# Performance work log

Measured on AMD Instinct MI355X. Metric: run time of the kernel, lower is better.

Reference implementation:

```python
import jax, jax.numpy as jnp
import numpy as np

COMMITMENT_COST = 0.25


def setup_inputs() -> dict:
    key = jax.random.key(0)
    k1, k2 = jax.random.split(key)
    x = jax.random.normal(k1, (32, 256, 32, 32), dtype=jnp.float32)          # NCHW latents
    embedding = jax.random.normal(k2, (1024, 256), dtype=jnp.float32)        # [K, D] codebook
    return {"x": x, "embedding": embedding}


def reference(x, embedding):
    # NCHW -> NHWC, flatten to [N, D]
    inp = jnp.transpose(x, (0, 2, 3, 1))
    B, H, W, D = inp.shape
    K = embedding.shape[0]
    flat = inp.reshape(-1, D)                                                # [N, D]

    dists = (jnp.sum(flat * flat, axis=1, keepdims=True)
             + jnp.sum(embedding * embedding, axis=1)
             - 2.0 * flat @ embedding.T)
    idx = jnp.argmin(dists, axis=1)                                          # [N]
    encodings = jax.nn.one_hot(idx, K, dtype=flat.dtype)                     # [N, K]

    quantized = (encodings @ embedding).reshape(B, H, W, D)

    # commitment loss (codebook detached, eval path: no EMA update)
    e_latent_loss = jnp.mean(jnp.square(jax.lax.stop_gradient(quantized) - inp))
    loss = COMMITMENT_COST * e_latent_loss

    # straight-through estimator
    quantized_st = inp + jax.lax.stop_gradient(quantized - inp)

    avg_probs = jnp.mean(encodings, axis=0)
    perplexity = jnp.exp(-jnp.sum(avg_probs * jnp.log(avg_probs + 1e-10)))

    return (loss, jnp.transpose(quantized_st, (0, 3, 1, 2)), perplexity, encodings)
```

## Files before the change

kernel.cpp:

```cpp
#include <hip/hip_runtime.h>
#include <math.h>

#define D    256
#define K    1024
#define HWX  1024
#define NPTS 32768
#define PT   64
#define NCHUNK 64

#define Q_OFF    1
#define PERP_OFF (1 + 8388608)
#define ENC_OFF  (2 + 8388608)

#define WS_FRAG_OFF 147456

typedef __attribute__((ext_vector_type(8))) short bf16x8;
typedef __attribute__((ext_vector_type(4))) float f32x4;
typedef __attribute__((ext_vector_type(2))) float f32x2;

__device__ __forceinline__ unsigned short bf16_rne(float f) {
  unsigned int u = __float_as_uint(f);
  u = u + 0x7fffu + ((u >> 16) & 1u);
  return (unsigned short)(u >> 16);
}

#define CONV(F, H, L)                                                          \
  {                                                                            \
    H = bf16_rne(F);                                                           \
    const float fh_ = __uint_as_float((unsigned)(H) << 16);                    \
    L = bf16_rne((F)-fh_);                                                     \
  }

__global__ __launch_bounds__(256) void vq_frag(const float* __restrict__ emb,
                                               unsigned int* __restrict__ frag,
                                               float* __restrict__ enorm,
                                               int* __restrict__ counts,
                                               float* __restrict__ loss_accum) {
  const int gid = blockIdx.x * 256 + threadIdx.x;
  const int c = gid >> 5, g = gid & 31;
  const float* src = emb + (size_t)c * D + g * 8;
  const float4 a = *(const float4*)src;
  const float4 b = *(const float4*)(src + 4);
  float s = a.x * a.x + a.y * a.y + a.z * a.z + a.w * a.w +
            b.x * b.x + b.y * b.y + b.z * b.z + b.w * b.w;
#pragma unroll
  for (int off = 1; off < 32; off <<= 1) s += __shfl_xor(s, off);
  if (g == 0) enorm[c] = s;
  unsigned short h0, h1, h2, h3, h4, h5, h6, h7;
  unsigned short l0, l1, l2, l3, l4, l5, l6, l7;
  CONV(a.x, h0, l0) CONV(a.y, h1, l1) CONV(a.z, h2, l2) CONV(a.w, h3, l3)
  CONV(b.x, h4, l4) CONV(b.y, h5, l5) CONV(b.z, h6, l6) CONV(b.w, h7, l7)
  uint4 uh, ul;
  uh.x = (unsigned)h0 | ((unsigned)h1 << 16); uh.y = (unsigned)h2 | ((unsigned)h3 << 16);
  uh.z = (unsigned)h4 | ((unsigned)h5 << 16); uh.w = (unsigned)h6 | ((unsigned)h7 << 16);
  ul.x = (unsigned)l0 | ((unsigned)l1 << 16); ul.y = (unsigned)l2 | ((unsigned)l3 << 16);
  ul.z = (unsigned)l4 | ((unsigned)l5 << 16); ul.w = (unsigned)l6 | ((unsigned)l7 << 16);
  const int fragidx = (c >> 4) * 16 + (g >> 2) * 2;
  const int Lo = ((c & 15) + 16 * (g & 3)) * 4;
  *(uint4*)(frag + (size_t)fragidx * 256 + Lo) = uh;
  *(uint4*)(frag + (size_t)(fragidx + 1) * 256 + Lo) = ul;
  if (gid < K) counts[gid] = 0;
  if (gid == 0) *loss_accum = 0.0f;
}

#define ISSUE_CHUNK(P, SEL)                                                    \
  {                                                                            \
    const unsigned* gsrc = fragg + (size_t)(P)*4096 + t * 4;                   \
    unsigned short* ldst = fbuf + (SEL)*8192 + t * 8;                          \
    _Pragma("unroll") for (int q = 0; q < 4; ++q)                              \
        __builtin_amdgcn_global_load_lds(                                      \
            (const __attribute__((address_space(1))) unsigned*)(gsrc + q * 1024), \
            (__attribute__((address_space(3))) unsigned*)(ldst + q * 2048),    \
            16, 0, 0);                                                         \
  }

#define AHOIST(KSv)                                                            \
  ah##KSv = *(const bf16x8*)&fbuf[((w * 4 + ((KSv)&3)) * 2 + 0) * 512 + lane * 8]; \
  al##KSv = *(const bf16x8*)&fbuf[((w * 4 + ((KSv)&3)) * 2 + 1) * 512 + lane * 8];

#define KS3(KSv)                                                               \
  {                                                                            \
    const bf16x8 bh = *(const bf16x8*)&fbuf[bufo + ((KSv)*2 + 0) * 512 + lane * 8]; \
    const bf16x8 bl = *(const bf16x8*)&fbuf[bufo + ((KSv)*2 + 1) * 512 + lane * 8]; \
    acc = __builtin_amdgcn_mfma_f32_16x16x32_bf16(ah##KSv, bh, acc, 0, 0, 0);  \
    acc = __builtin_amdgcn_mfma_f32_16x16x32_bf16(al##KSv, bh, acc, 0, 0, 0);  \
    acc = __builtin_amdgcn_mfma_f32_16x16x32_bf16(ah##KSv, bl, acc, 0, 0, 0);  \
  }

#define COMPUTE_CHUNK(P, BUFO)                                                 \
  {                                                                            \
    const int bufo = (BUFO);                                                   \
    f32x4 acc = {0.f, 0.f, 0.f, 0.f};                                          \
    KS3(0) KS3(1) KS3(2) KS3(3) KS3(4) KS3(5) KS3(6) KS3(7)                    \
    const int code = (P)*16 + (lane & 15);                                     \
    const float en_l = en_s[code];                                             \
    float m;                                                                   \
    m = en_l - 2.0f * acc[0]; if (m < mv[0]) { mv[0] = m; mi[0] = code; }      \
    m = en_l - 2.0f * acc[1]; if (m < mv[1]) { mv[1] = m; mi[1] = code; }      \
    m = en_l - 2.0f * acc[2]; if (m < mv[2]) { mv[2] = m; mi[2] = code; }      \
    m = en_l - 2.0f * acc[3]; if (m < mv[3]) { mv[3] = m; mi[3] = code; }      \
  }

#define ENC_ZERO(P)                                                            \
  {                                                                            \
    const f32x2 z_ = {0.f, 0.f};                                               \
    __builtin_nontemporal_store(z_, encz + (P)*512 + t);                       \
    __builtin_nontemporal_store(z_, encz + (P)*512 + 256 + t);                 \
  }

#define CFENCE asm volatile("" ::: "memory");

#define STAGE_X(H)                                                             \
  {                                                                            \
    const int pt = t & 63, cb_ = t >> 6;                                       \
    const float* xb = x + (size_t)bb * (D * HWX) + hw0 + pt;                   \
    _Pragma("unroll 8") for (int i = 0; i < 32; ++i) {                         \
      const int c = (H)*128 + cb_ + 4 * i;                                     \
      const float f = xb[(size_t)c * HWX];                                     \
      unsigned short h_, l_;                                                   \
      CONV(f, h_, l_)                                                          \
      xn_acc += f * f;                                                         \
      const int ksl = (c >> 5) & 3, quad = (c >> 3) & 3, j = c & 7;            \
      const int base =                                                         \
          (((pt >> 4) * 4 + ksl) * 2) * 512 + ((pt & 15) + 16 * quad) * 8 + j; \
      fbuf[base] = h_;                                                         \
      fbuf[base + 512] = l_;                                                   \
    }                                                                          \
  }

__global__ __launch_bounds__(256) void vq_main(const float* __restrict__ x,
                                               const unsigned int* __restrict__ fragg,
                                               const float* __restrict__ emb,
                                               const float* __restrict__ enorm,
                                               float* __restrict__ out_q,
                                               float* __restrict__ out_enc,
                                               float* __restrict__ loss_accum,
                                               int* __restrict__ counts) {
  __shared__ __align__(16) unsigned short fbuf[24576];
  __shared__ float en_s[K];
  __shared__ float xn_part[256];
  __shared__ float val_s[PT];
  __shared__ int idx_s[PT];

  const int t = threadIdx.x;
  const int lane = t & 63;
  const int w = t >> 6;
  const int p0 = blockIdx.x * PT;
  const int bb = p0 >> 10;
  const int hw0 = p0 & 1023;

  bf16x8 ah0, ah1, ah2, ah3, ah4, ah5, ah6, ah7;
  bf16x8 al0, al1, al2, al3, al4, al5, al6, al7;
  float xn_acc = 0.0f;

  STAGE_X(0)
  for (int i = t; i < K; i += 256) en_s[i] = enorm[i];
  __syncthreads();
  AHOIST(0) AHOIST(1) AHOIST(2) AHOIST(3)
  __syncthreads();
  STAGE_X(1)
  xn_part[t] = xn_acc;
  __syncthreads();
  AHOIST(4) AHOIST(5) AHOIST(6) AHOIST(7)
  __syncthreads();

  float mv[4];
  int mi[4];
#pragma unroll
  for (int i = 0; i < 4; ++i) { mv[i] = 3.4e38f; mi[i] = 0; }

  f32x2* encz = reinterpret_cast<f32x2*>(out_enc + (size_t)p0 * K);

  ISSUE_CHUNK(0, 0)
  CFENCE
  ISSUE_CHUNK(1, 1)
  asm volatile("s_waitcnt vmcnt(4)" ::: "memory");
  __builtin_amdgcn_s_barrier();
  CFENCE
  ENC_ZERO(0)
  CFENCE
  ISSUE_CHUNK(2, 2)
  CFENCE
  COMPUTE_CHUNK(0, 0)
  int cb = 1;
  for (int p = 1; p < NCHUNK - 1; ++p) {
    asm volatile("s_waitcnt vmcnt(6)" ::: "memory");
    __builtin_amdgcn_s_barrier();
    CFENCE
    ENC_ZERO(p)
    CFENCE
    if (p + 2 < NCHUNK) {
      ISSUE_CHUNK(p + 2, cb == 0 ? 2 : cb - 1)
    }
    CFENCE
    COMPUTE_CHUNK(p, cb * 8192)
    cb = cb == 2 ? 0 : cb + 1;
  }
  asm volatile("s_waitcnt vmcnt(2)" ::: "memory");
  __builtin_amdgcn_s_barrier();
  CFENCE
  ENC_ZERO(63)
  COMPUTE_CHUNK(63, 0)

#pragma unroll
  for (int off = 1; off < 16; off <<= 1) {
#pragma unroll
    for (int i = 0; i < 4; ++i) {
      const float ov = __shfl_xor(mv[i], off);
      const int oi = __shfl_xor(mi[i], off);
      if (ov < mv[i] || (ov == mv[i] && oi < mi[i])) { mv[i] = ov; mi[i] = oi; }
    }
  }
  if ((lane & 15) == 0) {
    const int quad = lane >> 4;
#pragma unroll
    for (int i = 0; i < 4; ++i) {
      val_s[w * 16 + quad * 4 + i] = mv[i];
      idx_s[w * 16 + quad * 4 + i] = mi[i];
    }
  }
  asm volatile("s_waitcnt vmcnt(0)" ::: "memory");
  __syncthreads();

  float dist = 0.0f;
  if (t < PT) {
    float xn = 0.0f;
#pragma unroll
    for (int g = 0; g < 4; ++g) xn += xn_part[t + 64 * g];
    dist = val_s[t] + xn;
    atomicAdd(&counts[idx_s[t]], 1);
    out_enc[(size_t)(p0 + t) * K + idx_s[t]] = 1.0f;
  }
  if (t < 64) {
#pragma unroll
    for (int off = 32; off > 0; off >>= 1) dist += __shfl_down(dist, off);
    if (t == 0) atomicAdd(loss_accum, dist);
  }

  float* xq = (float*)fbuf;
  for (int qd = 0; qd < 4; ++qd) {
    __syncthreads();
#pragma unroll
    for (int rr = 0; rr < 4; ++rr) {
      const int r = w * 4 + rr;
      const float4 v = ((const float4*)(emb + (size_t)idx_s[qd * 16 + r] * D))[lane];
      float* dst = &xq[r * 257 + lane];
      dst[0] = v.x; dst[64] = v.y; dst[128] = v.z; dst[192] = v.w;
    }
    __syncthreads();
    const int pt = t & 15;
    float* qb = out_q + (size_t)bb * D * HWX + hw0 + qd * 16 + pt;
#pragma unroll
    for (int ii = 0; ii < 16; ++ii) {
      const int ci = (t >> 4) + 16 * ii;
      const int pos = (ci >> 2) + 64 * (ci & 3);
      qb[(size_t)ci * HWX] = xq[pt * 257 + pos];
    }
  }
}

__global__ __launch_bounds__(256) void vq_final(const int* __restrict__ counts,
                                                const float* __restrict__ loss_accum,
                                                float* __restrict__ out) {
  __shared__ float sh[4];
  const int t = threadIdx.x;
  float s = 0.0f;
  for (int k = t; k < K; k += 256) {
    const float p = (float)counts[k] * (1.0f / 32768.0f);
    s += p * logf(p + 1e-10f);
  }
#pragma unroll
  for (int off = 32; off > 0; off >>= 1) s += __shfl_down(s, off);
  if ((t & 63) == 0) sh[t >> 6] = s;
  __syncthreads();
  if (t == 0) {
    const float tot = sh[0] + sh[1] + sh[2] + sh[3];
    out[PERP_OFF] = expf(-tot);
    out[0] = 0.25f * (*loss_accum) / 8388608.0f;
  }
}

extern "C" void kernel_launch(void* const* d_in, const int* in_sizes, int n_in,
                              void* d_out, int out_size, void* d_ws, size_t ws_size,
                              hipStream_t stream) {
  const float* x = (const float*)d_in[0];
  const float* emb = (const float*)d_in[1];
  float* out = (float*)d_out;
  float* enorm = (float*)d_ws;
  int* counts = (int*)((char*)d_ws + 4096);
  float* loss_accum = (float*)((char*)d_ws + 8192);
  unsigned int* fragg = (unsigned int*)((char*)d_ws + WS_FRAG_OFF);

  hipLaunchKernelGGL(vq_frag, dim3(128), dim3(256), 0, stream,
                     emb, fragg, enorm, counts, loss_accum);
  hipLaunchKernelGGL(vq_main, dim3(NPTS / PT), dim3(256), 0, stream,
                     x, fragg, emb, enorm, out + Q_OFF, out + ENC_OFF,
                     loss_accum, counts);
  hipLaunchKernelGGL(vq_final, dim3(1), dim3(256), 0, stream,
                     counts, loss_accum, out);
}
```

Baseline: 264.0 us.

## Halve block to two waves, each computing two 16-point tiles per B fragment

The main kernel now runs 128 threads (2 waves) per block instead of 256. Each wave owns two 16-point A tiles and reuses every codebook B fragment loaded from LDS for both tiles, interleaving two accumulators. This halves the LDS B-fragment reads per MFMA and adds independent MFMA chains. The cost is twice the A registers per thread and fewer waves to hide latency. The staging, prefetch, zeroing and epilogue loops and the vmcnt waits are rescaled to match.

```diff
diff --git a/kernel.cpp b/kernel.cpp
--- a/kernel.cpp
+++ b/kernel.cpp
@@ -67,45 +67,57 @@
   {                                                                            \
     const unsigned* gsrc = fragg + (size_t)(P)*4096 + t * 4;                   \
     unsigned short* ldst = fbuf + (SEL)*8192 + t * 8;                          \
-    _Pragma("unroll") for (int q = 0; q < 4; ++q)                              \
+    _Pragma("unroll") for (int q = 0; q < 8; ++q)                              \
         __builtin_amdgcn_global_load_lds(                                      \
-            (const __attribute__((address_space(1))) unsigned*)(gsrc + q * 1024), \
-            (__attribute__((address_space(3))) unsigned*)(ldst + q * 2048),    \
+            (const __attribute__((address_space(1))) unsigned*)(gsrc + q * 512), \
+            (__attribute__((address_space(3))) unsigned*)(ldst + q * 1024),    \
             16, 0, 0);                                                         \
   }
 
-#define AHOIST(KSv)                                                            \
-  ah##KSv = *(const bf16x8*)&fbuf[((w * 4 + ((KSv)&3)) * 2 + 0) * 512 + lane * 8]; \
-  al##KSv = *(const bf16x8*)&fbuf[((w * 4 + ((KSv)&3)) * 2 + 1) * 512 + lane * 8];
+#define AHOIST2(KSv)                                                           \
+  ahA##KSv = *(const bf16x8*)&fbuf[((tA * 4 + ((KSv)&3)) * 2 + 0) * 512 + lane * 8]; \
+  alA##KSv = *(const bf16x8*)&fbuf[((tA * 4 + ((KSv)&3)) * 2 + 1) * 512 + lane * 8]; \
+  ahB##KSv = *(const bf16x8*)&fbuf[((tB * 4 + ((KSv)&3)) * 2 + 0) * 512 + lane * 8]; \
+  alB##KSv = *(const bf16x8*)&fbuf[((tB * 4 + ((KSv)&3)) * 2 + 1) * 512 + lane * 8];
 
 #define KS3(KSv)                                                               \
   {                                                                            \
     const bf16x8 bh = *(const bf16x8*)&fbuf[bufo + ((KSv)*2 + 0) * 512 + lane * 8]; \
     const bf16x8 bl = *(const bf16x8*)&fbuf[bufo + ((KSv)*2 + 1) * 512 + lane * 8]; \
-    acc = __builtin_amdgcn_mfma_f32_16x16x32_bf16(ah##KSv, bh, acc, 0, 0, 0);  \
-    acc = __builtin_amdgcn_mfma_f32_16x16x32_bf16(al##KSv, bh, acc, 0, 0, 0);  \
-    acc = __builtin_amdgcn_mfma_f32_16x16x32_bf16(ah##KSv, bl, acc, 0, 0, 0);  \
+    accA = __builtin_amdgcn_mfma_f32_16x16x32_bf16(ahA##KSv, bh, accA, 0, 0, 0); \
+    accB = __builtin_amdgcn_mfma_f32_16x16x32_bf16(ahB##KSv, bh, accB, 0, 0, 0); \
+    accA = __builtin_amdgcn_mfma_f32_16x16x32_bf16(alA##KSv, bh, accA, 0, 0, 0); \
+    accB = __builtin_amdgcn_mfma_f32_16x16x32_bf16(alB##KSv, bh, accB, 0, 0, 0); \
+    accA = __builtin_amdgcn_mfma_f32_16x16x32_bf16(ahA##KSv, bl, accA, 0, 0, 0); \
+    accB = __builtin_amdgcn_mfma_f32_16x16x32_bf16(ahB##KSv, bl, accB, 0, 0, 0); \
   }
 
 #define COMPUTE_CHUNK(P, BUFO)                                                 \
   {                                                                            \
     const int bufo = (BUFO);                                                   \
-    f32x4 acc = {0.f, 0.f, 0.f, 0.f};                                          \
+    f32x4 accA = {0.f, 0.f, 0.f, 0.f};                                         \
+    f32x4 accB = {0.f, 0.f, 0.f, 0.f};                                         \
     KS3(0) KS3(1) KS3(2) KS3(3) KS3(4) KS3(5) KS3(6) KS3(7)                    \
     const int code = (P)*16 + (lane & 15);                                     \
     const float en_l = en_s[code];                                             \
     float m;                                                                   \
-    m = en_l - 2.0f * acc[0]; if (m < mv[0]) { mv[0] = m; mi[0] = code; }      \
-    m = en_l - 2.0f * acc[1]; if (m < mv[1]) { mv[1] = m; mi[1] = code; }      \
-    m = en_l - 2.0f * acc[2]; if (m < mv[2]) { mv[2] = m; mi[2] = code; }      \
-    m = en_l - 2.0f * acc[3]; if (m < mv[3]) { mv[3] = m; mi[3] = code; }      \
+    m = en_l - 2.0f * accA[0]; if (m < mvA[0]) { mvA[0] = m; miA[0] = code; }  \
+    m = en_l - 2.0f * accA[1]; if (m < mvA[1]) { mvA[1] = m; miA[1] = code; }  \
+    m = en_l - 2.0f * accA[2]; if (m < mvA[2]) { mvA[2] = m; miA[2] = code; }  \
+    m = en_l - 2.0f * accA[3]; if (m < mvA[3]) { mvA[3] = m; miA[3] = code; }  \
+    m = en_l - 2.0f * accB[0]; if (m < mvB[0]) { mvB[0] = m; miB[0] = code; }  \
+    m = en_l - 2.0f * accB[1]; if (m < mvB[1]) { mvB[1] = m; miB[1] = code; }  \
+    m = en_l - 2.0f * accB[2]; if (m < mvB[2]) { mvB[2] = m; miB[2] = code; }  \
+    m = en_l - 2.0f * accB[3]; if (m < mvB[3]) { mvB[3] = m; miB[3] = code; }  \
   }
 
 #define ENC_ZERO(P)                                                            \
   {                                                                            \
     const f32x2 z_ = {0.f, 0.f};                                               \
     __builtin_nontemporal_store(z_, encz + (P)*512 + t);                       \
+    __builtin_nontemporal_store(z_, encz + (P)*512 + 128 + t);                 \
     __builtin_nontemporal_store(z_, encz + (P)*512 + 256 + t);                 \
+    __builtin_nontemporal_store(z_, encz + (P)*512 + 384 + t);                 \
   }
 
 #define CFENCE asm volatile("" ::: "memory");
@@ -114,8 +126,8 @@
   {                                                                            \
     const int pt = t & 63, cb_ = t >> 6;                                       \
     const float* xb = x + (size_t)bb * (D * HWX) + hw0 + pt;                   \
-    _Pragma("unroll 8") for (int i = 0; i < 32; ++i) {                         \
-      const int c = (H)*128 + cb_ + 4 * i;                                     \
+    _Pragma("unroll 8") for (int i = 0; i < 64; ++i) {                         \
+      const int c = (H)*128 + cb_ + 2 * i;                                     \
       const float f = xb[(size_t)c * HWX];                                     \
       unsigned short h_, l_;                                                   \
       CONV(f, h_, l_)                                                          \
@@ -128,53 +140,58 @@
     }                                                                          \
   }
 
-__global__ __launch_bounds__(256) void vq_main(const float* __restrict__ x,
-                                               const unsigned int* __restrict__ fragg,
-                                               const float* __restrict__ emb,
-                                               const float* __restrict__ enorm,
-                                               float* __restrict__ out_q,
-                                               float* __restrict__ out_enc,
-                                               float* __restrict__ loss_accum,
-                                               int* __restrict__ counts) {
+__global__ __launch_bounds__(128, 1) void vq_main(const float* __restrict__ x,
+                                                  const unsigned int* __restrict__ fragg,
+                                                  const float* __restrict__ emb,
+                                                  const float* __restrict__ enorm,
+                                                  float* __restrict__ out_q,
+                                                  float* __restrict__ out_enc,
+                                                  float* __restrict__ loss_accum,
+                                                  int* __restrict__ counts) {
   __shared__ __align__(16) unsigned short fbuf[24576];
   __shared__ float en_s[K];
-  __shared__ float xn_part[256];
+  __shared__ float xn_part[128];
   __shared__ float val_s[PT];
   __shared__ int idx_s[PT];
 
   const int t = threadIdx.x;
   const int lane = t & 63;
   const int w = t >> 6;
+  const int tA = 2 * w, tB = 2 * w + 1;
   const int p0 = blockIdx.x * PT;
   const int bb = p0 >> 10;
   const int hw0 = p0 & 1023;
 
-  bf16x8 ah0, ah1, ah2, ah3, ah4, ah5, ah6, ah7;
-  bf16x8 al0, al1, al2, al3, al4, al5, al6, al7;
+  bf16x8 ahA0, ahA1, ahA2, ahA3, ahA4, ahA5, ahA6, ahA7;
+  bf16x8 alA0, alA1, alA2, alA3, alA4, alA5, alA6, alA7;
+  bf16x8 ahB0, ahB1, ahB2, ahB3, ahB4, ahB5, ahB6, ahB7;
+  bf16x8 alB0, alB1, alB2, alB3, alB4, alB5, alB6, alB7;
   float xn_acc = 0.0f;
 
   STAGE_X(0)
-  for (int i = t; i < K; i += 256) en_s[i] = enorm[i];
-  __syncthreads();
-  AHOIST(0) AHOIST(1) AHOIST(2) AHOIST(3)
+  for (int i = t; i < K; i += 128) en_s[i] = enorm[i];
+  __syncthreads();
+  AHOIST2(0) AHOIST2(1) AHOIST2(2) AHOIST2(3)
   __syncthreads();
   STAGE_X(1)
   xn_part[t] = xn_acc;
   __syncthreads();
-  AHOIST(4) AHOIST(5) AHOIST(6) AHOIST(7)
-  __syncthreads();
-
-  float mv[4];
-  int mi[4];
-#pragma unroll
-  for (int i = 0; i < 4; ++i) { mv[i] = 3.4e38f; mi[i] = 0; }
+  AHOIST2(4) AHOIST2(5) AHOIST2(6) AHOIST2(7)
+  __syncthreads();
+
+  float mvA[4], mvB[4];
+  int miA[4], miB[4];
+#pragma unroll
+  for (int i = 0; i < 4; ++i) {
+    mvA[i] = 3.4e38f; miA[i] = 0; mvB[i] = 3.4e38f; miB[i] = 0;
+  }
 
   f32x2* encz = reinterpret_cast<f32x2*>(out_enc + (size_t)p0 * K);
 
   ISSUE_CHUNK(0, 0)
   CFENCE
   ISSUE_CHUNK(1, 1)
-  asm volatile("s_waitcnt vmcnt(4)" ::: "memory");
+  asm volatile("s_waitcnt vmcnt(8)" ::: "memory");
   __builtin_amdgcn_s_barrier();
   CFENCE
   ENC_ZERO(0)
@@ -184,7 +201,7 @@
   COMPUTE_CHUNK(0, 0)
   int cb = 1;
   for (int p = 1; p < NCHUNK - 1; ++p) {
-    asm volatile("s_waitcnt vmcnt(6)" ::: "memory");
+    asm volatile("s_waitcnt vmcnt(12)" ::: "memory");
     __builtin_amdgcn_s_barrier();
     CFENCE
     ENC_ZERO(p)
@@ -196,7 +213,7 @@
     COMPUTE_CHUNK(p, cb * 8192)
     cb = cb == 2 ? 0 : cb + 1;
   }
-  asm volatile("s_waitcnt vmcnt(2)" ::: "memory");
+  asm volatile("s_waitcnt vmcnt(4)" ::: "memory");
   __builtin_amdgcn_s_barrier();
   CFENCE
   ENC_ZERO(63)
@@ -206,17 +223,21 @@
   for (int off = 1; off < 16; off <<= 1) {
 #pragma unroll
     for (int i = 0; i < 4; ++i) {
-      const float ov = __shfl_xor(mv[i], off);
-      const int oi = __shfl_xor(mi[i], off);
-      if (ov < mv[i] || (ov == mv[i] && oi < mi[i])) { mv[i] = ov; mi[i] = oi; }
+      float ov; int oi;
+      ov = __shfl_xor(mvA[i], off); oi = __shfl_xor(miA[i], off);
+      if (ov < mvA[i] || (ov == mvA[i] && oi < miA[i])) { mvA[i] = ov; miA[i] = oi; }
+      ov = __shfl_xor(mvB[i], off); oi = __shfl_xor(miB[i], off);
+      if (ov < mvB[i] || (ov == mvB[i] && oi < miB[i])) { mvB[i] = ov; miB[i] = oi; }
     }
   }
   if ((lane & 15) == 0) {
     const int quad = lane >> 4;
 #pragma unroll
     for (int i = 0; i < 4; ++i) {
-      val_s[w * 16 + quad * 4 + i] = mv[i];
-      idx_s[w * 16 + quad * 4 + i] = mi[i];
+      val_s[tA * 16 + quad * 4 + i] = mvA[i];
+      idx_s[tA * 16 + quad * 4 + i] = miA[i];
+      val_s[tB * 16 + quad * 4 + i] = mvB[i];
+      idx_s[tB * 16 + quad * 4 + i] = miB[i];
     }
   }
   asm volatile("s_waitcnt vmcnt(0)" ::: "memory");
@@ -224,9 +245,7 @@
 
   float dist = 0.0f;
   if (t < PT) {
-    float xn = 0.0f;
-#pragma unroll
-    for (int g = 0; g < 4; ++g) xn += xn_part[t + 64 * g];
+    const float xn = xn_part[t] + xn_part[t + 64];
     dist = val_s[t] + xn;
     atomicAdd(&counts[idx_s[t]], 1);
     out_enc[(size_t)(p0 + t) * K + idx_s[t]] = 1.0f;
@@ -241,8 +260,8 @@
   for (int qd = 0; qd < 4; ++qd) {
     __syncthreads();
 #pragma unroll
-    for (int rr = 0; rr < 4; ++rr) {
-      const int r = w * 4 + rr;
+    for (int rr = 0; rr < 8; ++rr) {
+      const int r = w * 8 + rr;
       const float4 v = ((const float4*)(emb + (size_t)idx_s[qd * 16 + r] * D))[lane];
       float* dst = &xq[r * 257 + lane];
       dst[0] = v.x; dst[64] = v.y; dst[128] = v.z; dst[192] = v.w;
@@ -251,8 +270,8 @@
     const int pt = t & 15;
     float* qb = out_q + (size_t)bb * D * HWX + hw0 + qd * 16 + pt;
 #pragma unroll
-    for (int ii = 0; ii < 16; ++ii) {
-      const int ci = (t >> 4) + 16 * ii;
+    for (int ii = 0; ii < 32; ++ii) {
+      const int ci = (t >> 4) + 8 * ii;
       const int pos = (ci >> 2) + 64 * (ci & 3);
       qb[(size_t)ci * HWX] = xq[pt * 257 + pos];
     }
@@ -293,7 +312,7 @@
 
   hipLaunchKernelGGL(vq_frag, dim3(128), dim3(256), 0, stream,
                      emb, fragg, enorm, counts, loss_accum);
-  hipLaunchKernelGGL(vq_main, dim3(NPTS / PT), dim3(256), 0, stream,
+  hipLaunchKernelGGL(vq_main, dim3(NPTS / PT), dim3(128), 0, stream,
                      x, fragg, emb, enorm, out + Q_OFF, out + ENC_OFF,
                      loss_accum, counts);
   hipLaunchKernelGGL(vq_final, dim3(1), dim3(256), 0, stream,
```

Result: slower. 284.3 us (+7.7%).

## Halve points per block and split codebook chunks across wave pairs

Applied to the files above, without the earlier changes.

Each block now handles 32 points instead of 64, so there are twice as many blocks. The four waves are split into two point-tiles times two codebook-parity groups: each wave pair computes alternate 16-code chunks, and the partial argmins are merged through shared memory. The x staging becomes a single pass with no intermediate barrier, and the ||x||^2 sum is added to the loss directly via atomics. The aim is more parallelism and occupancy across CUs. The cost is that every block re-streams the full codebook fragments for half as many points, doubling global/L2 codebook traffic, and adds more atomics.

```diff
diff --git a/kernel.cpp b/kernel.cpp
--- a/kernel.cpp
+++ b/kernel.cpp
@@ -5,7 +5,7 @@
 #define K    1024
 #define HWX  1024
 #define NPTS 32768
-#define PT   64
+#define PT   32
 #define NCHUNK 64
 
 #define Q_OFF    1
@@ -75,8 +75,8 @@
   }
 
 #define AHOIST(KSv)                                                            \
-  ah##KSv = *(const bf16x8*)&fbuf[((w * 4 + ((KSv)&3)) * 2 + 0) * 512 + lane * 8]; \
-  al##KSv = *(const bf16x8*)&fbuf[((w * 4 + ((KSv)&3)) * 2 + 1) * 512 + lane * 8];
+  ah##KSv = *(const bf16x8*)&fbuf[((tw * 8 + (KSv)) * 2 + 0) * 512 + lane * 8]; \
+  al##KSv = *(const bf16x8*)&fbuf[((tw * 8 + (KSv)) * 2 + 1) * 512 + lane * 8];
 
 #define KS3(KSv)                                                               \
   {                                                                            \
@@ -104,29 +104,10 @@
 #define ENC_ZERO(P)                                                            \
   {                                                                            \
     const f32x2 z_ = {0.f, 0.f};                                               \
-    __builtin_nontemporal_store(z_, encz + (P)*512 + t);                       \
-    __builtin_nontemporal_store(z_, encz + (P)*512 + 256 + t);                 \
+    __builtin_nontemporal_store(z_, encz + (P)*256 + t);                       \
   }
 
 #define CFENCE asm volatile("" ::: "memory");
-
-#define STAGE_X(H)                                                             \
-  {                                                                            \
-    const int pt = t & 63, cb_ = t >> 6;                                       \
-    const float* xb = x + (size_t)bb * (D * HWX) + hw0 + pt;                   \
-    _Pragma("unroll 8") for (int i = 0; i < 32; ++i) {                         \
-      const int c = (H)*128 + cb_ + 4 * i;                                     \
-      const float f = xb[(size_t)c * HWX];                                     \
-      unsigned short h_, l_;                                                   \
-      CONV(f, h_, l_)                                                          \
-      xn_acc += f * f;                                                         \
-      const int ksl = (c >> 5) & 3, quad = (c >> 3) & 3, j = c & 7;            \
-      const int base =                                                         \
-          (((pt >> 4) * 4 + ksl) * 2) * 512 + ((pt & 15) + 16 * quad) * 8 + j; \
-      fbuf[base] = h_;                                                         \
-      fbuf[base + 512] = l_;                                                   \
-    }                                                                          \
-  }
 
 __global__ __launch_bounds__(256) void vq_main(const float* __restrict__ x,
                                                const unsigned int* __restrict__ fragg,
@@ -138,13 +119,15 @@
                                                int* __restrict__ counts) {
   __shared__ __align__(16) unsigned short fbuf[24576];
   __shared__ float en_s[K];
-  __shared__ float xn_part[256];
-  __shared__ float val_s[PT];
   __shared__ int idx_s[PT];
+  __shared__ float wv_s[4][16];
+  __shared__ int wi_s[4][16];
 
   const int t = threadIdx.x;
   const int lane = t & 63;
   const int w = t >> 6;
+  const int tw = w & 1;
+  const int pw = w >> 1;
   const int p0 = blockIdx.x * PT;
   const int bb = p0 >> 10;
   const int hw0 = p0 & 1023;
@@ -153,14 +136,26 @@
   bf16x8 al0, al1, al2, al3, al4, al5, al6, al7;
   float xn_acc = 0.0f;
 
-  STAGE_X(0)
+  {
+    const int pt = t & 31, cb_ = t >> 5;
+    const float* xb = x + (size_t)bb * (D * HWX) + hw0 + pt;
+#pragma unroll 8
+    for (int i = 0; i < 32; ++i) {
+      const int c = cb_ + 8 * i;
+      const float f = xb[(size_t)c * HWX];
+      unsigned short h_, l_;
+      CONV(f, h_, l_)
+      xn_acc += f * f;
+      const int ks = c >> 5, quad = (c >> 3) & 3, j = c & 7;
+      const int base =
+          (((pt >> 4) * 8 + ks) * 2) * 512 + ((pt & 15) + 16 * quad) * 8 + j;
+      fbuf[base] = h_;
+      fbuf[base + 512] = l_;
+    }
+  }
   for (int i = t; i < K; i += 256) en_s[i] = enorm[i];
   __syncthreads();
   AHOIST(0) AHOIST(1) AHOIST(2) AHOIST(3)
-  __syncthreads();
-  STAGE_X(1)
-  xn_part[t] = xn_acc;
-  __syncthreads();
   AHOIST(4) AHOIST(5) AHOIST(6) AHOIST(7)
   __syncthreads();
 
@@ -181,10 +176,10 @@
   CFENCE
   ISSUE_CHUNK(2, 2)
   CFENCE
-  COMPUTE_CHUNK(0, 0)
+  if (pw == 0) COMPUTE_CHUNK(0, 0)
   int cb = 1;
   for (int p = 1; p < NCHUNK - 1; ++p) {
-    asm volatile("s_waitcnt vmcnt(6)" ::: "memory");
+    asm volatile("s_waitcnt vmcnt(5)" ::: "memory");
     __builtin_amdgcn_s_barrier();
     CFENCE
     ENC_ZERO(p)
@@ -193,14 +188,14 @@
       ISSUE_CHUNK(p + 2, cb == 0 ? 2 : cb - 1)
     }
     CFENCE
-    COMPUTE_CHUNK(p, cb * 8192)
+    if ((p & 1) == pw) COMPUTE_CHUNK(p, cb * 8192)
     cb = cb == 2 ? 0 : cb + 1;
   }
-  asm volatile("s_waitcnt vmcnt(2)" ::: "memory");
+  asm volatile("s_waitcnt vmcnt(1)" ::: "memory");
   __builtin_amdgcn_s_barrier();
   CFENCE
   ENC_ZERO(63)
-  COMPUTE_CHUNK(63, 0)
+  if (pw == 1) COMPUTE_CHUNK(63, 0)
 
 #pragma unroll
   for (int off = 1; off < 16; off <<= 1) {
@@ -215,37 +210,47 @@
     const int quad = lane >> 4;
 #pragma unroll
     for (int i = 0; i < 4; ++i) {
-      val_s[w * 16 + quad * 4 + i] = mv[i];
-      idx_s[w * 16 + quad * 4 + i] = mi[i];
-    }
+      wv_s[w][quad * 4 + i] = mv[i];
+      wi_s[w][quad * 4 + i] = mi[i];
+    }
+  }
+  {
+    float xs = xn_acc;
+#pragma unroll
+    for (int off = 32; off > 0; off >>= 1) xs += __shfl_down(xs, off);
+    if (lane == 0) atomicAdd(loss_accum, xs);
   }
   asm volatile("s_waitcnt vmcnt(0)" ::: "memory");
   __syncthreads();
 
-  float dist = 0.0f;
+  float v = 0.0f;
   if (t < PT) {
-    float xn = 0.0f;
-#pragma unroll
-    for (int g = 0; g < 4; ++g) xn += xn_part[t + 64 * g];
-    dist = val_s[t] + xn;
-    atomicAdd(&counts[idx_s[t]], 1);
-    out_enc[(size_t)(p0 + t) * K + idx_s[t]] = 1.0f;
-  }
-  if (t < 64) {
-#pragma unroll
-    for (int off = 32; off > 0; off >>= 1) dist += __shfl_down(dist, off);
-    if (t == 0) atomicAdd(loss_accum, dist);
-  }
+    const int tl = t >> 4, li = t & 15;
+    const float vA = wv_s[tl][li], vB = wv_s[tl + 2][li];
+    const int iA = wi_s[tl][li], iB = wi_s[tl + 2][li];
+    int ix;
+    if (vB < vA || (vB == vA && iB < iA)) { v = vB; ix = iB; }
+    else { v = vA; ix = iA; }
+    idx_s[t] = ix;
+    atomicAdd(&counts[ix], 1);
+    out_enc[(size_t)(p0 + t) * K + ix] = 1.0f;
+  }
+  if (w == 0) {
+#pragma unroll
+    for (int off = 32; off > 0; off >>= 1) v += __shfl_down(v, off);
+    if (lane == 0) atomicAdd(loss_accum, v);
+  }
+  __syncthreads();
 
   float* xq = (float*)fbuf;
-  for (int qd = 0; qd < 4; ++qd) {
+  for (int qd = 0; qd < 2; ++qd) {
     __syncthreads();
 #pragma unroll
     for (int rr = 0; rr < 4; ++rr) {
       const int r = w * 4 + rr;
-      const float4 v = ((const float4*)(emb + (size_t)idx_s[qd * 16 + r] * D))[lane];
+      const float4 vv = ((const float4*)(emb + (size_t)idx_s[qd * 16 + r] * D))[lane];
       float* dst = &xq[r * 257 + lane];
-      dst[0] = v.x; dst[64] = v.y; dst[128] = v.z; dst[192] = v.w;
+      dst[0] = vv.x; dst[64] = vv.y; dst[128] = vv.z; dst[192] = vv.w;
     }
     __syncthreads();
     const int pt = t & 15;
```

Result: slower. 349.5 us (+32.4%).

## Switch codebook streaming to double-buffered 32-code pairs with dual accumulators

Applied to the files above, without the earlier changes.

Replaces the three-slot ring of 16-code chunks with a two-slot double buffer that holds 32-code pairs. Each pair is computed with two independent MFMA accumulator chains interleaved, to give the matrix units more independent work. This halves the number of barriers and waitcnt points per block, and the encoding-zero stores are batched per pair. In exchange, prefetch depth drops from two chunks ahead to one, and the LDS buffer grows from 48 KB to 64 KB, which may lower the number of blocks resident per CU.

```diff
diff --git a/kernel.cpp b/kernel.cpp
--- a/kernel.cpp
+++ b/kernel.cpp
@@ -6,7 +6,7 @@
 #define HWX  1024
 #define NPTS 32768
 #define PT   64
-#define NCHUNK 64
+#define NPAIR 32
 
 #define Q_OFF    1
 #define PERP_OFF (1 + 8388608)
@@ -63,11 +63,11 @@
   if (gid == 0) *loss_accum = 0.0f;
 }
 
-#define ISSUE_CHUNK(P, SEL)                                                    \
-  {                                                                            \
-    const unsigned* gsrc = fragg + (size_t)(P)*4096 + t * 4;                   \
-    unsigned short* ldst = fbuf + (SEL)*8192 + t * 8;                          \
-    _Pragma("unroll") for (int q = 0; q < 4; ++q)                              \
+#define ISSUE_PAIR(P, HALF)                                                    \
+  {                                                                            \
+    const unsigned* gsrc = fragg + (size_t)(P)*8192 + t * 4;                   \
+    unsigned short* ldst = fbuf + (HALF)*16384 + t * 8;                        \
+    _Pragma("unroll") for (int q = 0; q < 8; ++q)                              \
         __builtin_amdgcn_global_load_lds(                                      \
             (const __attribute__((address_space(1))) unsigned*)(gsrc + q * 1024), \
             (__attribute__((address_space(3))) unsigned*)(ldst + q * 2048),    \
@@ -78,34 +78,50 @@
   ah##KSv = *(const bf16x8*)&fbuf[((w * 4 + ((KSv)&3)) * 2 + 0) * 512 + lane * 8]; \
   al##KSv = *(const bf16x8*)&fbuf[((w * 4 + ((KSv)&3)) * 2 + 1) * 512 + lane * 8];
 
-#define KS3(KSv)                                                               \
-  {                                                                            \
-    const bf16x8 bh = *(const bf16x8*)&fbuf[bufo + ((KSv)*2 + 0) * 512 + lane * 8]; \
-    const bf16x8 bl = *(const bf16x8*)&fbuf[bufo + ((KSv)*2 + 1) * 512 + lane * 8]; \
-    acc = __builtin_amdgcn_mfma_f32_16x16x32_bf16(ah##KSv, bh, acc, 0, 0, 0);  \
-    acc = __builtin_amdgcn_mfma_f32_16x16x32_bf16(al##KSv, bh, acc, 0, 0, 0);  \
-    acc = __builtin_amdgcn_mfma_f32_16x16x32_bf16(ah##KSv, bl, acc, 0, 0, 0);  \
-  }
-
-#define COMPUTE_CHUNK(P, BUFO)                                                 \
-  {                                                                            \
-    const int bufo = (BUFO);                                                   \
-    f32x4 acc = {0.f, 0.f, 0.f, 0.f};                                          \
-    KS3(0) KS3(1) KS3(2) KS3(3) KS3(4) KS3(5) KS3(6) KS3(7)                    \
-    const int code = (P)*16 + (lane & 15);                                     \
-    const float en_l = en_s[code];                                             \
+#define KS3G(KSv, ACC, BUFO)                                                   \
+  {                                                                            \
+    const bf16x8 bh = *(const bf16x8*)&fbuf[(BUFO) + ((KSv)*2 + 0) * 512 + lane * 8]; \
+    const bf16x8 bl = *(const bf16x8*)&fbuf[(BUFO) + ((KSv)*2 + 1) * 512 + lane * 8]; \
+    ACC = __builtin_amdgcn_mfma_f32_16x16x32_bf16(ah##KSv, bh, ACC, 0, 0, 0);  \
+    ACC = __builtin_amdgcn_mfma_f32_16x16x32_bf16(al##KSv, bh, ACC, 0, 0, 0);  \
+    ACC = __builtin_amdgcn_mfma_f32_16x16x32_bf16(ah##KSv, bl, ACC, 0, 0, 0);  \
+  }
+
+#define COMPUTE_PAIR(I)                                                        \
+  {                                                                            \
+    const int b0 = ((I)&1) * 16384;                                            \
+    const int b1 = b0 + 8192;                                                  \
+    f32x4 acc0 = {0.f, 0.f, 0.f, 0.f};                                         \
+    f32x4 acc1 = {0.f, 0.f, 0.f, 0.f};                                         \
+    KS3G(0, acc0, b0) KS3G(0, acc1, b1)                                        \
+    KS3G(1, acc0, b0) KS3G(1, acc1, b1)                                        \
+    KS3G(2, acc0, b0) KS3G(2, acc1, b1)                                        \
+    KS3G(3, acc0, b0) KS3G(3, acc1, b1)                                        \
+    KS3G(4, acc0, b0) KS3G(4, acc1, b1)                                        \
+    KS3G(5, acc0, b0) KS3G(5, acc1, b1)                                        \
+    KS3G(6, acc0, b0) KS3G(6, acc1, b1)                                        \
+    KS3G(7, acc0, b0) KS3G(7, acc1, b1)                                        \
+    const int c0 = (I)*32 + (lane & 15);                                       \
+    const int c1 = c0 + 16;                                                    \
+    const float e0 = en_s[c0], e1 = en_s[c1];                                  \
     float m;                                                                   \
-    m = en_l - 2.0f * acc[0]; if (m < mv[0]) { mv[0] = m; mi[0] = code; }      \
-    m = en_l - 2.0f * acc[1]; if (m < mv[1]) { mv[1] = m; mi[1] = code; }      \
-    m = en_l - 2.0f * acc[2]; if (m < mv[2]) { mv[2] = m; mi[2] = code; }      \
-    m = en_l - 2.0f * acc[3]; if (m < mv[3]) { mv[3] = m; mi[3] = code; }      \
-  }
-
-#define ENC_ZERO(P)                                                            \
+    m = e0 - 2.0f * acc0[0]; if (m < mv[0]) { mv[0] = m; mi[0] = c0; }         \
+    m = e0 - 2.0f * acc0[1]; if (m < mv[1]) { mv[1] = m; mi[1] = c0; }         \
+    m = e0 - 2.0f * acc0[2]; if (m < mv[2]) { mv[2] = m; mi[2] = c0; }         \
+    m = e0 - 2.0f * acc0[3]; if (m < mv[3]) { mv[3] = m; mi[3] = c0; }         \
+    m = e1 - 2.0f * acc1[0]; if (m < mv[0]) { mv[0] = m; mi[0] = c1; }         \
+    m = e1 - 2.0f * acc1[1]; if (m < mv[1]) { mv[1] = m; mi[1] = c1; }         \
+    m = e1 - 2.0f * acc1[2]; if (m < mv[2]) { mv[2] = m; mi[2] = c1; }         \
+    m = e1 - 2.0f * acc1[3]; if (m < mv[3]) { mv[3] = m; mi[3] = c1; }         \
+  }
+
+#define ENC_ZERO2(I)                                                           \
   {                                                                            \
     const f32x2 z_ = {0.f, 0.f};                                               \
-    __builtin_nontemporal_store(z_, encz + (P)*512 + t);                       \
-    __builtin_nontemporal_store(z_, encz + (P)*512 + 256 + t);                 \
+    __builtin_nontemporal_store(z_, encz + (I)*1024 + t);                      \
+    __builtin_nontemporal_store(z_, encz + (I)*1024 + 256 + t);                \
+    __builtin_nontemporal_store(z_, encz + (I)*1024 + 512 + t);                \
+    __builtin_nontemporal_store(z_, encz + (I)*1024 + 768 + t);                \
   }
 
 #define CFENCE asm volatile("" ::: "memory");
@@ -136,7 +152,7 @@
                                                float* __restrict__ out_enc,
                                                float* __restrict__ loss_accum,
                                                int* __restrict__ counts) {
-  __shared__ __align__(16) unsigned short fbuf[24576];
+  __shared__ __align__(16) unsigned short fbuf[32768];
   __shared__ float en_s[K];
   __shared__ float xn_part[256];
   __shared__ float val_s[PT];
@@ -171,36 +187,22 @@
 
   f32x2* encz = reinterpret_cast<f32x2*>(out_enc + (size_t)p0 * K);
 
-  ISSUE_CHUNK(0, 0)
+  ISSUE_PAIR(0, 0)
+  asm volatile("s_waitcnt vmcnt(0)" ::: "memory");
+  __builtin_amdgcn_s_barrier();
+  for (int i = 0; i < NPAIR - 1; ++i) {
+    CFENCE
+    ISSUE_PAIR(i + 1, (i + 1) & 1)
+    CFENCE
+    ENC_ZERO2(i)
+    CFENCE
+    COMPUTE_PAIR(i)
+    asm volatile("s_waitcnt vmcnt(4)" ::: "memory");
+    __builtin_amdgcn_s_barrier();
+  }
   CFENCE
-  ISSUE_CHUNK(1, 1)
-  asm volatile("s_waitcnt vmcnt(4)" ::: "memory");
-  __builtin_amdgcn_s_barrier();
-  CFENCE
-  ENC_ZERO(0)
-  CFENCE
-  ISSUE_CHUNK(2, 2)
-  CFENCE
-  COMPUTE_CHUNK(0, 0)
-  int cb = 1;
-  for (int p = 1; p < NCHUNK - 1; ++p) {
-    asm volatile("s_waitcnt vmcnt(6)" ::: "memory");
-    __builtin_amdgcn_s_barrier();
-    CFENCE
-    ENC_ZERO(p)
-    CFENCE
-    if (p + 2 < NCHUNK) {
-      ISSUE_CHUNK(p + 2, cb == 0 ? 2 : cb - 1)
-    }
-    CFENCE
-    COMPUTE_CHUNK(p, cb * 8192)
-    cb = cb == 2 ? 0 : cb + 1;
-  }
-  asm volatile("s_waitcnt vmcnt(2)" ::: "memory");
-  __builtin_amdgcn_s_barrier();
-  CFENCE
-  ENC_ZERO(63)
-  COMPUTE_CHUNK(63, 0)
+  ENC_ZERO2(NPAIR - 1)
+  COMPUTE_PAIR(NPAIR - 1)
 
 #pragma unroll
   for (int off = 1; off < 16; off <<= 1) {
```

Measured after the change: 249.6 us. -5.5%, faster.
